# Kernel optimization log

Hardware: AMD Instinct MI355X
Metric: run time of the kernel (lower is better)

## Reference

```python
import jax, jax.numpy as jnp
import numpy as np

H = 64  # lstm hidden

def _lstm_scan(xs, h0, c0, wih, whh, bih, bhh):
    # xs: [T,B,D]; torch gate order i,f,g,o
    def step(carry, xt):
        h, c = carry
        gates = xt @ wih.T + h @ whh.T + bih + bhh
        i, f, g, o = jnp.split(gates, 4, axis=-1)
        c = jax.nn.sigmoid(f) * c + jax.nn.sigmoid(i) * jnp.tanh(g)
        h = jax.nn.sigmoid(o) * jnp.tanh(c)
        return (h, c), h
    (h, c), hs = jax.lax.scan(step, (h0, c0), xs)
    return hs, h, c


def setup_inputs() -> dict:
    key = jax.random.key(0)
    ks = jax.random.split(key, 32)
    r = lambda i, shape: (jax.random.normal(ks[i], shape, jnp.float32) * 0.05)
    B, T = 2048, 128
    inp = {
        "x": jax.random.normal(ks[0], (B, T, 37), jnp.float32),
        "enc_lin_w": r(1, (64, 37)), "enc_lin_b": r(2, (64,)),
        "enc_wih_f": r(3, (4 * H, 64)), "enc_whh_f": r(4, (4 * H, H)),
        "enc_bih_f": r(5, (4 * H,)), "enc_bhh_f": r(6, (4 * H,)),
        "enc_wih_b": r(7, (4 * H, 64)), "enc_whh_b": r(8, (4 * H, H)),
        "enc_bih_b": r(9, (4 * H,)), "enc_bhh_b": r(10, (4 * H,)),
        "att1_w": r(11, (32, 192)), "att1_b": r(12, (32,)),
        "att2_w": r(13, (1, 32)), "att2_b": r(14, (1,)),
        "dec_wih": r(15, (4 * H, 128)), "dec_whh": r(16, (4 * H, H)),
        "dec_bih": r(17, (4 * H,)), "dec_bhh": r(18, (4 * H,)),
        "dec_lin_w": r(19, (11, H)), "dec_lin_b": r(20, (11,)),
        "output_len": 10,
    }
    return inp


def reference(x, enc_lin_w, enc_lin_b,
              enc_wih_f, enc_whh_f, enc_bih_f, enc_bhh_f,
              enc_wih_b, enc_whh_b, enc_bih_b, enc_bhh_b,
              att1_w, att1_b, att2_w, att2_b,
              dec_wih, dec_whh, dec_bih, dec_bhh,
              dec_lin_w, dec_lin_b, output_len):
    B, T, _ = x.shape
    # ---- Encoder: linear -> relu -> BiLSTM ----
    e = jax.nn.relu(x @ enc_lin_w.T + enc_lin_b)          # [B,T,64]
    xs = jnp.transpose(e, (1, 0, 2))                       # [T,B,64]
    z = jnp.zeros((B, H), x.dtype)
    hf, _, _ = _lstm_scan(xs, z, z, enc_wih_f, enc_whh_f, enc_bih_f, enc_bhh_f)
    hb, _, _ = _lstm_scan(xs[::-1], z, z, enc_wih_b, enc_whh_b, enc_bih_b, enc_bhh_b)
    feats = jnp.concatenate([hf, hb[::-1]], axis=-1)       # [T,B,128]
    feats = jnp.transpose(feats, (1, 0, 2))                # [B,T,128]

    # ---- Decoder loop with (degenerate) additive attention ----
    def dec_step(carry, _):
        h, c = carry
        h_rep = jnp.broadcast_to(h[:, None, :], (B, T, H))
        fin = jnp.concatenate([feats, h_rep], axis=-1)     # [B,T,192]
        a = jnp.tanh(fin @ att1_w.T + att1_b)              # [B,T,32]
        s = a @ att2_w.T + att2_b                          # [B,T,1]
        scores = jax.nn.softmax(s, axis=-1)                # all ones (faithful to source)
        fd = jnp.sum(feats * scores, axis=1)               # [B,128]
        gates = fd @ dec_wih.T + h @ dec_whh.T + dec_bih + dec_bhh
        i, f, g, o = jnp.split(gates, 4, axis=-1)
        c = jax.nn.sigmoid(f) * c + jax.nn.sigmoid(i) * jnp.tanh(g)
        h = jax.nn.sigmoid(o) * jnp.tanh(c)
        out = jax.nn.softmax(h @ dec_lin_w.T + dec_lin_b, axis=-1)  # [B,11]
        return (h, c), out

    (_, _), outs = jax.lax.scan(dec_step, (z, z), None, length=output_len)
    return jnp.transpose(outs, (1, 0, 2))                  # [B,output_len,11]
```

## Files before the change

### kernel.cpp

```cpp
#include <hip/hip_runtime.h>


typedef _Float16 f16;
typedef f16 f16x8 __attribute__((ext_vector_type(8)));
typedef f16 f16x4 __attribute__((ext_vector_type(4)));
typedef float f32x4 __attribute__((ext_vector_type(4)));

#define MFMA16(a, b, c) __builtin_amdgcn_mfma_f32_16x16x32_f16(a, b, c, 0, 0, 0)

#define NLOG2E  -1.4426950408889634f
#define N2LOG2E -2.8853900817779268f

__device__ __forceinline__ float rcp_(float x) { return __builtin_amdgcn_rcpf(x); }
__device__ __forceinline__ float ex2_(float x) { return __builtin_amdgcn_exp2f(x); }
__device__ __forceinline__ float sigf(float x) { return 1.f / (1.f + __expf(-x)); }
__device__ __forceinline__ float tanhf_fast(float x) {
  float e = __expf(2.f * x);
  return 1.f - 2.f / (e + 1.f);
}


#define TC 8
__global__ __launch_bounds__(256) void enc_linear_k(
    const float* __restrict__ x, const float* __restrict__ w1,
    const float* __restrict__ b1, f16* __restrict__ efrag) {
  const int bg = blockIdx.x;
  const int tc = blockIdx.y;
  const int tid = threadIdx.x;
  const int w = tid >> 6, l = tid & 63;
  const int rho = l & 15, c = l >> 4;

  __shared__ float xls[16][8 * 37 + 1];
  __shared__ float ldsw[64 * 37];
  __shared__ __align__(16) f16 fstage[TC][2][64][8];

  for (int i = tid; i < 64 * 37; i += 256) ldsw[i] = w1[i];
#pragma unroll
  for (int rr = 0; rr < 4; rr++) {
    const int r = w * 4 + rr;
    const float* src = x + ((size_t)(bg * 16 + r) * 128 + tc * TC) * 37;
    for (int e = l; e < 296; e += 64) xls[r][e] = src[e];
  }
  __syncthreads();

  f16x8 a0, a1;
  {
    const float* pw = ldsw + (16 * w + rho) * 37;
#pragma unroll
    for (int i = 0; i < 8; i++) a0[i] = (f16)pw[8 * c + i];
#pragma unroll
    for (int i = 0; i < 8; i++) a1[i] = (f16)((c == 0 && i < 5) ? pw[32 + i] : 0.f);
  }
  f32x4 bias;
#pragma unroll
  for (int r = 0; r < 4; r++) bias[r] = b1[16 * w + 4 * c + r];

#pragma unroll
  for (int tl = 0; tl < TC; tl++) {
    const float* px = &xls[rho][tl * 37];
    f16x8 xb0, xb1;
#pragma unroll
    for (int i = 0; i < 8; i++) xb0[i] = (f16)px[8 * c + i];
#pragma unroll
    for (int i = 0; i < 8; i++) xb1[i] = (f16)((c == 0 && i < 5) ? px[32 + i] : 0.f);
    f32x4 acc = bias;
    acc = MFMA16(a0, xb0, acc);
    acc = MFMA16(a1, xb1, acc);
    f16x4 pk;
#pragma unroll
    for (int r = 0; r < 4; r++) pk[r] = (f16)fmaxf(acc[r], 0.f);
    const int d0 = 16 * w + 4 * c;
    *(f16x4*)&fstage[tl][w >> 1][rho | (((d0 >> 3) & 3) << 4)][d0 & 7] = pk;
  }
  __syncthreads();

  const float4* srcf = (const float4*)fstage;
  float4* dstf = (float4*)efrag;
  for (int i = tid; i < TC * 2 * 64; i += 256) {
    const int tl = i >> 7, rest = i & 127;
    dstf[((size_t)((tc * TC + tl) * 128 + bg) * 2) * 64 + rest] = srcf[i];
  }
}

__global__ __launch_bounds__(512, 2) void bilstm_k(
    const f16* __restrict__ efrag,
    const float* __restrict__ wih_f, const float* __restrict__ whh_f,
    const float* __restrict__ bih_f, const float* __restrict__ bhh_f,
    const float* __restrict__ wih_b, const float* __restrict__ whh_b,
    const float* __restrict__ bih_b, const float* __restrict__ bhh_b,
    float* __restrict__ fd) {
  const int bid = blockIdx.x;
  const int dir = bid >> 7;
  const int bg = bid & 127;
  const int tid = threadIdx.x;
  const int w = tid >> 6, l = tid & 63;
  const int rho = l & 15, c = l >> 4;
  const int gate = rho & 3, uoff = rho >> 2;

  const float* wih = dir ? wih_b : wih_f;
  const float* whh = dir ? whh_b : whh_f;
  const float* bih = dir ? bih_b : bih_f;
  const float* bhh = dir ? bhh_b : bhh_f;

  __shared__ __align__(16) f16 hbuf[2][2][64][8];
  {
    int* hz = (int*)hbuf;
    for (int i = tid; i < (int)(sizeof(hbuf) / 4); i += 512) hz[i] = 0;
  }

  const float sA = (gate == 2) ? N2LOG2E : NLOG2E;

  f16x8 aih[2][2], ahh[2][2];
#pragma unroll
  for (int q = 0; q < 2; q++) {
    const int m = 2 * w + q;
    const int n = gate * 64 + 4 * m + uoff;
#pragma unroll
    for (int ks = 0; ks < 2; ks++) {
      const float* p1 = wih + n * 64 + ks * 32 + c * 8;
      const float* p2 = whh + n * 64 + ks * 32 + c * 8;
      f16x8 v1, v2;
#pragma unroll
      for (int i = 0; i < 8; i++) {
        v1[i] = (f16)(p1[i] * sA);
        v2[i] = (f16)(p2[i] * sA);
      }
      aih[q][ks] = v1;
      ahh[q][ks] = v2;
    }
  }
  f32x4 bias[2];
#pragma unroll
  for (int q = 0; q < 2; q++) {
    const int j = 8 * w + 4 * q + c;
#pragma unroll
    for (int r = 0; r < 4; r++) {
      const float sr = (r == 2) ? N2LOG2E : NLOG2E;
      bias[q][r] = (bih[64 * r + j] + bhh[64 * r + j]) * sr;
    }
  }

  const f16x8* eb = (const f16x8*)efrag;
#define EIDX(t) (((size_t)(((dir ? 127 - (t) : (t)) * 128) + bg) * 2) * 64 + l)
  f16x8 ec0 = eb[EIDX(0)], ec1 = eb[EIDX(0) + 64];
  f16x8 e10 = eb[EIDX(1)], e11 = eb[EIDX(1) + 64];
  f16x8 e20 = eb[EIDX(2)], e21 = eb[EIDX(2) + 64];

  float cst[2] = {0.f, 0.f};
  float hs[2] = {0.f, 0.f};

  __syncthreads();

#pragma unroll 4
  for (int t = 0; t < 128; t++) {
    const int cur = t & 1;
    const int t3 = (t + 3 < 128) ? t + 3 : 127;
    const f16x8 ld0 = eb[EIDX(t3)];
    const f16x8 ld1 = eb[EIDX(t3) + 64];

    f16x8 h0 = *(const f16x8*)&hbuf[cur][0][l][0];
    f16x8 h1 = *(const f16x8*)&hbuf[cur][1][l][0];
#pragma unroll
    for (int q = 0; q < 2; q++) {
      f32x4 a = bias[q];
      a = MFMA16(aih[q][0], ec0, a);
      a = MFMA16(aih[q][1], ec1, a);
      a = MFMA16(ahh[q][0], h0, a);
      a = MFMA16(ahh[q][1], h1, a);
      const float ig = rcp_(1.f + ex2_(a[0]));
      const float fg = rcp_(1.f + ex2_(a[1]));
      const float gg = 2.f * rcp_(1.f + ex2_(a[2])) - 1.f;
      const float og = rcp_(1.f + ex2_(a[3]));
      cst[q] = fg * cst[q] + ig * gg;
      const float th = 2.f * rcp_(1.f + ex2_(cst[q] * N2LOG2E)) - 1.f;
      const float h = og * th;
      hs[q] += h;
      const int j = 8 * w + 4 * q + c;
      hbuf[cur ^ 1][j >> 5][rho | (((j >> 3) & 3) << 4)][j & 7] = (f16)h;
    }
    ec0 = e10; ec1 = e11;
    e10 = e20; e11 = e21;
    e20 = ld0; e21 = ld1;
    asm volatile("s_waitcnt lgkmcnt(0)\n\ts_barrier" ::: "memory");
  }
#undef EIDX
#pragma unroll
  for (int q = 0; q < 2; q++) {
    const int j = 8 * w + 4 * q + c;
    fd[(size_t)(bg * 16 + rho) * 128 + dir * 64 + j] = hs[q];
  }
}

__global__ __launch_bounds__(256) void decoder_k(
    const float* __restrict__ fd,
    const float* __restrict__ dwih, const float* __restrict__ dwhh,
    const float* __restrict__ dbih, const float* __restrict__ dbhh,
    const float* __restrict__ dlw, const float* __restrict__ dlb,
    const int* __restrict__ outlen_p, float* __restrict__ out) {
  const int b0 = blockIdx.x * 16;
  const int tid = threadIdx.x;
  const int w = tid >> 6, l = tid & 63;
  const int rho = l & 15, c = l >> 4;
  const int gate = rho & 3, uoff = rho >> 2;
  const int outlen = *outlen_p;

  __shared__ __align__(16) f16 hbuf[2][2][64][8];
  __shared__ float h32[64][16];
  __shared__ float ldslw[11 * 64];
  __shared__ float ldslb[16];
  __shared__ float lg[16][16];

  {
    int* hz = (int*)hbuf;
    for (int i = tid; i < (int)(sizeof(hbuf) / 4); i += 256) hz[i] = 0;
  }
  for (int i = tid; i < 704; i += 256) ldslw[i] = dlw[i];
  if (tid < 16) ldslb[tid] = (tid < 11) ? dlb[tid] : 0.f;

  f16x8 awhh[4][2];
  f32x4 acc0[4];
  {
    f16x8 bfd[4];
#pragma unroll
    for (int ks = 0; ks < 4; ks++) {
      const float* p = fd + (size_t)(b0 + rho) * 128 + ks * 32 + c * 8;
      f16x8 v;
#pragma unroll
      for (int i = 0; i < 8; i++) v[i] = (f16)p[i];
      bfd[ks] = v;
    }
#pragma unroll
    for (int q = 0; q < 4; q++) {
      const int m = 4 * w + q;
      const int n = gate * 64 + 4 * m + uoff;
      f32x4 a;
      const int j = 16 * w + 4 * q + c;
#pragma unroll
      for (int r = 0; r < 4; r++) a[r] = dbih[64 * r + j] + dbhh[64 * r + j];
#pragma unroll
      for (int ks = 0; ks < 4; ks++) {
        const float* p = dwih + n * 128 + ks * 32 + c * 8;
        f16x8 v;
#pragma unroll
        for (int i = 0; i < 8; i++) v[i] = (f16)p[i];
        a = MFMA16(v, bfd[ks], a);
      }
      acc0[q] = a;
#pragma unroll
      for (int ks = 0; ks < 2; ks++) {
        const float* p = dwhh + n * 64 + ks * 32 + c * 8;
        f16x8 v;
#pragma unroll
        for (int i = 0; i < 8; i++) v[i] = (f16)p[i];
        awhh[q][ks] = v;
      }
    }
  }
  float cst[4] = {0.f, 0.f, 0.f, 0.f};
  __syncthreads();

  for (int s = 0; s < outlen; s++) {
    const int cur = s & 1;
    f16x8 h0 = *(const f16x8*)&hbuf[cur][0][l][0];
    f16x8 h1 = *(const f16x8*)&hbuf[cur][1][l][0];
#pragma unroll
    for (int q = 0; q < 4; q++) {
      f32x4 a = acc0[q];
      a = MFMA16(awhh[q][0], h0, a);
      a = MFMA16(awhh[q][1], h1, a);
      const float ig = sigf(a[0]);
      const float fg = sigf(a[1]);
      const float gg = tanhf_fast(a[2]);
      const float og = sigf(a[3]);
      cst[q] = fg * cst[q] + ig * gg;
      const float h = og * tanhf_fast(cst[q]);
      const int j = 16 * w + 4 * q + c;
      hbuf[cur ^ 1][j >> 5][rho | (((j >> 3) & 3) << 4)][j & 7] = (f16)h;
      h32[j][rho] = h;
    }
    __syncthreads();
    const int b = tid >> 4, o = tid & 15;
    float logit = 0.f;
    if (o < 11) {
      logit = ldslb[o];
      for (int jj = 0; jj < 64; jj++) logit += h32[jj][b] * ldslw[o * 64 + jj];
      lg[b][o] = logit;
    }
    __syncthreads();
    if (o < 11) {
      float mx = lg[b][0];
      for (int k = 1; k < 11; k++) mx = fmaxf(mx, lg[b][k]);
      float sum = 0.f;
      for (int k = 0; k < 11; k++) sum += __expf(lg[b][k] - mx);
      out[(size_t)(b0 + b) * outlen * 11 + (size_t)s * 11 + o] =
          __expf(logit - mx) / sum;
    }
    __syncthreads();
  }
}

extern "C" void kernel_launch(void* const* d_in, const int* in_sizes, int n_in,
                              void* d_out, int out_size, void* d_ws, size_t ws_size,
                              hipStream_t stream) {
  const float* x = (const float*)d_in[0];
  const float* w1 = (const float*)d_in[1];
  const float* b1 = (const float*)d_in[2];
  const float* wih_f = (const float*)d_in[3];
  const float* whh_f = (const float*)d_in[4];
  const float* bih_f = (const float*)d_in[5];
  const float* bhh_f = (const float*)d_in[6];
  const float* wih_b = (const float*)d_in[7];
  const float* whh_b = (const float*)d_in[8];
  const float* bih_b = (const float*)d_in[9];
  const float* bhh_b = (const float*)d_in[10];
  const float* dwih = (const float*)d_in[15];
  const float* dwhh = (const float*)d_in[16];
  const float* dbih = (const float*)d_in[17];
  const float* dbhh = (const float*)d_in[18];
  const float* dlw = (const float*)d_in[19];
  const float* dlb = (const float*)d_in[20];
  const int* outlen = (const int*)d_in[21];
  float* out = (float*)d_out;

  f16* efrag = (f16*)d_ws;
  float* fd = (float*)((char*)d_ws + (size_t)33554432);

  hipLaunchKernelGGL(enc_linear_k, dim3(128, 16), dim3(256), 0, stream,
                     x, w1, b1, efrag);
  hipLaunchKernelGGL(bilstm_k, dim3(256), dim3(512), 0, stream,
                     efrag, wih_f, whh_f, bih_f, bhh_f,
                     wih_b, whh_b, bih_b, bhh_b, fd);
  hipLaunchKernelGGL(decoder_k, dim3(128), dim3(256), 0, stream,
                     fd, dwih, dwhh, dbih, dbhh, dlw, dlb, outlen, out);
}
```

Baseline: 136.6 us.

## Fuse encoder linear into BiLSTM kernel with producer warps feeding LDS

Removes the separate encoder-linear kernel and its fp16 global intermediate. The fused kernel stages each batch group's full input slab in LDS. Four extra warps compute the linear+ReLU projection for step t+1 into a double-buffered LDS tile while eight LSTM warps consume step t. The LSTM gate MFMAs are also split into two independent accumulation chains to shorten the dependency chain. The costs are a large up-front LDS fill, higher LDS use per block that may reduce occupancy, and a scalar tail for the five leftover input features.

```diff
diff --git a/kernel.cpp b/kernel.cpp
--- a/kernel.cpp
+++ b/kernel.cpp
@@ -19,71 +19,9 @@
   return 1.f - 2.f / (e + 1.f);
 }
 
-
-#define TC 8
-__global__ __launch_bounds__(256) void enc_linear_k(
+__global__ __launch_bounds__(768, 3) void bilstm_fused_k(
     const float* __restrict__ x, const float* __restrict__ w1,
-    const float* __restrict__ b1, f16* __restrict__ efrag) {
-  const int bg = blockIdx.x;
-  const int tc = blockIdx.y;
-  const int tid = threadIdx.x;
-  const int w = tid >> 6, l = tid & 63;
-  const int rho = l & 15, c = l >> 4;
-
-  __shared__ float xls[16][8 * 37 + 1];
-  __shared__ float ldsw[64 * 37];
-  __shared__ __align__(16) f16 fstage[TC][2][64][8];
-
-  for (int i = tid; i < 64 * 37; i += 256) ldsw[i] = w1[i];
-#pragma unroll
-  for (int rr = 0; rr < 4; rr++) {
-    const int r = w * 4 + rr;
-    const float* src = x + ((size_t)(bg * 16 + r) * 128 + tc * TC) * 37;
-    for (int e = l; e < 296; e += 64) xls[r][e] = src[e];
-  }
-  __syncthreads();
-
-  f16x8 a0, a1;
-  {
-    const float* pw = ldsw + (16 * w + rho) * 37;
-#pragma unroll
-    for (int i = 0; i < 8; i++) a0[i] = (f16)pw[8 * c + i];
-#pragma unroll
-    for (int i = 0; i < 8; i++) a1[i] = (f16)((c == 0 && i < 5) ? pw[32 + i] : 0.f);
-  }
-  f32x4 bias;
-#pragma unroll
-  for (int r = 0; r < 4; r++) bias[r] = b1[16 * w + 4 * c + r];
-
-#pragma unroll
-  for (int tl = 0; tl < TC; tl++) {
-    const float* px = &xls[rho][tl * 37];
-    f16x8 xb0, xb1;
-#pragma unroll
-    for (int i = 0; i < 8; i++) xb0[i] = (f16)px[8 * c + i];
-#pragma unroll
-    for (int i = 0; i < 8; i++) xb1[i] = (f16)((c == 0 && i < 5) ? px[32 + i] : 0.f);
-    f32x4 acc = bias;
-    acc = MFMA16(a0, xb0, acc);
-    acc = MFMA16(a1, xb1, acc);
-    f16x4 pk;
-#pragma unroll
-    for (int r = 0; r < 4; r++) pk[r] = (f16)fmaxf(acc[r], 0.f);
-    const int d0 = 16 * w + 4 * c;
-    *(f16x4*)&fstage[tl][w >> 1][rho | (((d0 >> 3) & 3) << 4)][d0 & 7] = pk;
-  }
-  __syncthreads();
-
-  const float4* srcf = (const float4*)fstage;
-  float4* dstf = (float4*)efrag;
-  for (int i = tid; i < TC * 2 * 64; i += 256) {
-    const int tl = i >> 7, rest = i & 127;
-    dstf[((size_t)((tc * TC + tl) * 128 + bg) * 2) * 64 + rest] = srcf[i];
-  }
-}
-
-__global__ __launch_bounds__(512, 2) void bilstm_k(
-    const f16* __restrict__ efrag,
+    const float* __restrict__ b1,
     const float* __restrict__ wih_f, const float* __restrict__ whh_f,
     const float* __restrict__ bih_f, const float* __restrict__ bhh_f,
     const float* __restrict__ wih_b, const float* __restrict__ whh_b,
@@ -97,97 +35,146 @@
   const int rho = l & 15, c = l >> 4;
   const int gate = rho & 3, uoff = rho >> 2;
 
-  const float* wih = dir ? wih_b : wih_f;
-  const float* whh = dir ? whh_b : whh_f;
-  const float* bih = dir ? bih_b : bih_f;
-  const float* bhh = dir ? bhh_b : bhh_f;
-
+  __shared__ __align__(16) f16 xfrag[128][64][8];
   __shared__ __align__(16) f16 hbuf[2][2][64][8];
+  __shared__ __align__(16) f16 ebuf[2][2][64][8];
+  __shared__ f16 xtail[128][16][5];
+
   {
+    const float4* xsrc = (const float4*)(x + (size_t)bg * 16 * 4736);
+    for (int cidx = tid; cidx < 18944; cidx += 768) {
+      const float4 v = xsrc[cidx];
+      const int bb = ((cidx >> 5) * 56680) >> 21;
+      const int f0 = (cidx - bb * 1184) * 4;
+      const float vv[4] = {v.x, v.y, v.z, v.w};
+#pragma unroll
+      for (int e = 0; e < 4; e++) {
+        const int f = f0 + e;
+        const int tt = (f * 56680) >> 21;
+        const int kk = f - tt * 37;
+        const f16 hv = (f16)vv[e];
+        if (kk < 32) xfrag[tt][bb | (((kk >> 3) & 3) << 4)][kk & 7] = hv;
+        else xtail[tt][bb][kk - 32] = hv;
+      }
+    }
     int* hz = (int*)hbuf;
-    for (int i = tid; i < (int)(sizeof(hbuf) / 4); i += 512) hz[i] = 0;
-  }
-
-  const float sA = (gate == 2) ? N2LOG2E : NLOG2E;
-
+    for (int i = tid; i < 1024; i += 768) hz[i] = 0;
+  }
+
+  const bool enc = (w < 4);
+  f16x8 w1a = {};
+  float w1t[4][5];
+  f32x4 eb0 = {};
   f16x8 aih[2][2], ahh[2][2];
-#pragma unroll
-  for (int q = 0; q < 2; q++) {
-    const int m = 2 * w + q;
-    const int n = gate * 64 + 4 * m + uoff;
-#pragma unroll
-    for (int ks = 0; ks < 2; ks++) {
-      const float* p1 = wih + n * 64 + ks * 32 + c * 8;
-      const float* p2 = whh + n * 64 + ks * 32 + c * 8;
-      f16x8 v1, v2;
-#pragma unroll
-      for (int i = 0; i < 8; i++) {
-        v1[i] = (f16)(p1[i] * sA);
-        v2[i] = (f16)(p2[i] * sA);
-      }
-      aih[q][ks] = v1;
-      ahh[q][ks] = v2;
-    }
-  }
   f32x4 bias[2];
-#pragma unroll
-  for (int q = 0; q < 2; q++) {
-    const int j = 8 * w + 4 * q + c;
+
+  if (enc) {
+    const float* pw = w1 + (16 * w + rho) * 37;
+#pragma unroll
+    for (int i = 0; i < 8; i++) w1a[i] = (f16)pw[8 * c + i];
 #pragma unroll
     for (int r = 0; r < 4; r++) {
-      const float sr = (r == 2) ? N2LOG2E : NLOG2E;
-      bias[q][r] = (bih[64 * r + j] + bhh[64 * r + j]) * sr;
-    }
-  }
-
-  const f16x8* eb = (const f16x8*)efrag;
-#define EIDX(t) (((size_t)(((dir ? 127 - (t) : (t)) * 128) + bg) * 2) * 64 + l)
-  f16x8 ec0 = eb[EIDX(0)], ec1 = eb[EIDX(0) + 64];
-  f16x8 e10 = eb[EIDX(1)], e11 = eb[EIDX(1) + 64];
-  f16x8 e20 = eb[EIDX(2)], e21 = eb[EIDX(2) + 64];
+      const float* pt = w1 + (16 * w + 4 * c + r) * 37 + 32;
+#pragma unroll
+      for (int i = 0; i < 5; i++) w1t[r][i] = pt[i];
+      eb0[r] = b1[16 * w + 4 * c + r];
+    }
+  } else {
+    const int wr = w - 4;
+    const float* wih = dir ? wih_b : wih_f;
+    const float* whh = dir ? whh_b : whh_f;
+    const float* bih = dir ? bih_b : bih_f;
+    const float* bhh = dir ? bhh_b : bhh_f;
+    const float sA = (gate == 2) ? N2LOG2E : NLOG2E;
+#pragma unroll
+    for (int q = 0; q < 2; q++) {
+      const int m = 2 * wr + q;
+      const int n = gate * 64 + 4 * m + uoff;
+#pragma unroll
+      for (int ks = 0; ks < 2; ks++) {
+        const float* p1 = wih + n * 64 + ks * 32 + c * 8;
+        const float* p2 = whh + n * 64 + ks * 32 + c * 8;
+        f16x8 v1, v2;
+#pragma unroll
+        for (int i = 0; i < 8; i++) {
+          v1[i] = (f16)(p1[i] * sA);
+          v2[i] = (f16)(p2[i] * sA);
+        }
+        aih[q][ks] = v1;
+        ahh[q][ks] = v2;
+      }
+      const int j = 8 * wr + 4 * q + c;
+#pragma unroll
+      for (int r = 0; r < 4; r++) {
+        const float sr = (r == 2) ? N2LOG2E : NLOG2E;
+        bias[q][r] = (bih[64 * r + j] + bhh[64 * r + j]) * sr;
+      }
+    }
+  }
+
+  auto enc_build = [&](int tm, int buf) {
+    const f16x8 xb0 = *(const f16x8*)&xfrag[tm][l][0];
+    float xt[5];
+#pragma unroll
+    for (int i = 0; i < 5; i++) xt[i] = (float)xtail[tm][rho][i];
+    f32x4 ea = MFMA16(w1a, xb0, eb0);
+#pragma unroll
+    for (int r = 0; r < 4; r++)
+#pragma unroll
+      for (int i = 0; i < 5; i++) ea[r] += w1t[r][i] * xt[i];
+    f16x4 pk;
+#pragma unroll
+    for (int r = 0; r < 4; r++) pk[r] = (f16)fmaxf(ea[r], 0.f);
+    const int d0 = 16 * w + 4 * c;
+    *(f16x4*)&ebuf[buf][w >> 1][rho | (((d0 >> 3) & 3) << 4)][d0 & 7] = pk;
+  };
+
+  __syncthreads();
+
+  if (enc) enc_build(dir ? 127 : 0, 0);
+  __syncthreads();
 
   float cst[2] = {0.f, 0.f};
   float hs[2] = {0.f, 0.f};
-
-  __syncthreads();
-
-#pragma unroll 4
+  const f32x4 z4 = {0.f, 0.f, 0.f, 0.f};
+
   for (int t = 0; t < 128; t++) {
-    const int cur = t & 1;
-    const int t3 = (t + 3 < 128) ? t + 3 : 127;
-    const f16x8 ld0 = eb[EIDX(t3)];
-    const f16x8 ld1 = eb[EIDX(t3) + 64];
-
-    f16x8 h0 = *(const f16x8*)&hbuf[cur][0][l][0];
-    f16x8 h1 = *(const f16x8*)&hbuf[cur][1][l][0];
+    const int cur = t & 1, nxt = cur ^ 1;
+    if (enc) {
+      if (t + 1 < 128) enc_build(dir ? 126 - t : t + 1, nxt);
+    } else {
+      const f16x8 e0 = *(const f16x8*)&ebuf[cur][0][l][0];
+      const f16x8 e1 = *(const f16x8*)&ebuf[cur][1][l][0];
+      const f16x8 h0 = *(const f16x8*)&hbuf[cur][0][l][0];
+      const f16x8 h1 = *(const f16x8*)&hbuf[cur][1][l][0];
+#pragma unroll
+      for (int q = 0; q < 2; q++) {
+        f32x4 a1 = MFMA16(aih[q][0], e0, bias[q]);
+        f32x4 a2 = MFMA16(aih[q][1], e1, z4);
+        a1 = MFMA16(ahh[q][0], h0, a1);
+        a2 = MFMA16(ahh[q][1], h1, a2);
+        const f32x4 a = a1 + a2;
+        const float ig = rcp_(1.f + ex2_(a[0]));
+        const float fg = rcp_(1.f + ex2_(a[1]));
+        const float gg = 2.f * rcp_(1.f + ex2_(a[2])) - 1.f;
+        const float og = rcp_(1.f + ex2_(a[3]));
+        cst[q] = fg * cst[q] + ig * gg;
+        const float th = 2.f * rcp_(1.f + ex2_(cst[q] * N2LOG2E)) - 1.f;
+        const float h = og * th;
+        hs[q] += h;
+        const int j = 8 * (w - 4) + 4 * q + c;
+        hbuf[nxt][j >> 5][rho | (((j >> 3) & 3) << 4)][j & 7] = (f16)h;
+      }
+    }
+    asm volatile("s_waitcnt lgkmcnt(0)\n\ts_barrier" ::: "memory");
+  }
+
+  if (!enc) {
 #pragma unroll
     for (int q = 0; q < 2; q++) {
-      f32x4 a = bias[q];
-      a = MFMA16(aih[q][0], ec0, a);
-      a = MFMA16(aih[q][1], ec1, a);
-      a = MFMA16(ahh[q][0], h0, a);
-      a = MFMA16(ahh[q][1], h1, a);
-      const float ig = rcp_(1.f + ex2_(a[0]));
-      const float fg = rcp_(1.f + ex2_(a[1]));
-      const float gg = 2.f * rcp_(1.f + ex2_(a[2])) - 1.f;
-      const float og = rcp_(1.f + ex2_(a[3]));
-      cst[q] = fg * cst[q] + ig * gg;
-      const float th = 2.f * rcp_(1.f + ex2_(cst[q] * N2LOG2E)) - 1.f;
-      const float h = og * th;
-      hs[q] += h;
-      const int j = 8 * w + 4 * q + c;
-      hbuf[cur ^ 1][j >> 5][rho | (((j >> 3) & 3) << 4)][j & 7] = (f16)h;
-    }
-    ec0 = e10; ec1 = e11;
-    e10 = e20; e11 = e21;
-    e20 = ld0; e21 = ld1;
-    asm volatile("s_waitcnt lgkmcnt(0)\n\ts_barrier" ::: "memory");
-  }
-#undef EIDX
-#pragma unroll
-  for (int q = 0; q < 2; q++) {
-    const int j = 8 * w + 4 * q + c;
-    fd[(size_t)(bg * 16 + rho) * 128 + dir * 64 + j] = hs[q];
+      const int j = 8 * (w - 4) + 4 * q + c;
+      fd[(size_t)(bg * 16 + rho) * 128 + dir * 64 + j] = hs[q];
+    }
   }
 }
 
@@ -322,13 +309,10 @@
   const int* outlen = (const int*)d_in[21];
   float* out = (float*)d_out;
 
-  f16* efrag = (f16*)d_ws;
-  float* fd = (float*)((char*)d_ws + (size_t)33554432);
-
-  hipLaunchKernelGGL(enc_linear_k, dim3(128, 16), dim3(256), 0, stream,
-                     x, w1, b1, efrag);
-  hipLaunchKernelGGL(bilstm_k, dim3(256), dim3(512), 0, stream,
-                     efrag, wih_f, whh_f, bih_f, bhh_f,
+  float* fd = (float*)d_ws;
+
+  hipLaunchKernelGGL(bilstm_fused_k, dim3(256), dim3(768), 0, stream,
+                     x, w1, b1, wih_f, whh_f, bih_f, bhh_f,
                      wih_b, whh_b, bih_b, bhh_b, fd);
   hipLaunchKernelGGL(decoder_k, dim3(128), dim3(256), 0, stream,
                      fd, dwih, dwhh, dbih, dbhh, dlw, dlb, outlen, out);
```

New measurement: 142.3 us. +4.2%, slower.

## Restructure encoder linear tiling and split LSTM MFMA accumulation chains

Applied to the files above, without the earlier changes.

The encoder linear kernel now processes 32 timesteps per block instead of 8, loading x with float4 reads into an f16 LDS tile. Each wave keeps all four weight fragments in registers and computes the 5-element K tail with scalar FMAs instead of a second mostly-zero MFMA. In the BiLSTM recurrence, the four dependent MFMAs per gate group are split into two independent chains that are summed at the end, shortening the serial dependency on the critical recurrent path. The trade-offs are fewer encoder blocks (less parallelism), more register pressure, and an extra vector add per step.

```diff
diff --git a/kernel.cpp b/kernel.cpp
--- a/kernel.cpp
+++ b/kernel.cpp
@@ -20,7 +20,7 @@
 }
 
 
-#define TC 8
+#define XSTRIDE 1304
 __global__ __launch_bounds__(256) void enc_linear_k(
     const float* __restrict__ x, const float* __restrict__ w1,
     const float* __restrict__ b1, f16* __restrict__ efrag) {
@@ -30,55 +30,77 @@
   const int w = tid >> 6, l = tid & 63;
   const int rho = l & 15, c = l >> 4;
 
-  __shared__ float xls[16][8 * 37 + 1];
-  __shared__ float ldsw[64 * 37];
-  __shared__ __align__(16) f16 fstage[TC][2][64][8];
-
-  for (int i = tid; i < 64 * 37; i += 256) ldsw[i] = w1[i];
-#pragma unroll
-  for (int rr = 0; rr < 4; rr++) {
-    const int r = w * 4 + rr;
-    const float* src = x + ((size_t)(bg * 16 + r) * 128 + tc * TC) * 37;
-    for (int e = l; e < 296; e += 64) xls[r][e] = src[e];
+  __shared__ f16 xls[16 * XSTRIDE];
+  __shared__ __align__(16) f16 fstage[32][2][64][8];
+
+  {
+    const float4* xsrc =
+        (const float4*)(x + ((size_t)(bg * 16) * 128 + tc * 32) * 37);
+    for (int cidx = tid; cidx < 16 * 296; cidx += 256) {
+      const int r = cidx / 296;
+      const int f4 = cidx - r * 296;
+      const float4 v = xsrc[(size_t)r * 1184 + f4];
+      const float vv[4] = {v.x, v.y, v.z, v.w};
+      const int f0 = f4 * 4;
+#pragma unroll
+      for (int e = 0; e < 4; e++) {
+        const int f = f0 + e;
+        const int t = (f * 1772) >> 16;
+        const int k = f - t * 37;
+        xls[r * XSTRIDE + t * 40 + k] = (f16)vv[e];
+      }
+    }
+  }
+
+  f16x8 w1a[4];
+  float w1t[4][4][5];
+  f32x4 ebias[4];
+#pragma unroll
+  for (int m = 0; m < 4; m++) {
+    const float* pw = w1 + (16 * m + rho) * 37;
+    f16x8 v0;
+#pragma unroll
+    for (int i = 0; i < 8; i++) v0[i] = (f16)pw[8 * c + i];
+    w1a[m] = v0;
+#pragma unroll
+    for (int r = 0; r < 4; r++) {
+      const float* pt = w1 + (16 * m + 4 * c + r) * 37 + 32;
+#pragma unroll
+      for (int i = 0; i < 5; i++) w1t[m][r][i] = pt[i];
+      ebias[m][r] = b1[16 * m + 4 * c + r];
+    }
   }
   __syncthreads();
 
-  f16x8 a0, a1;
-  {
-    const float* pw = ldsw + (16 * w + rho) * 37;
-#pragma unroll
-    for (int i = 0; i < 8; i++) a0[i] = (f16)pw[8 * c + i];
-#pragma unroll
-    for (int i = 0; i < 8; i++) a1[i] = (f16)((c == 0 && i < 5) ? pw[32 + i] : 0.f);
-  }
-  f32x4 bias;
-#pragma unroll
-  for (int r = 0; r < 4; r++) bias[r] = b1[16 * w + 4 * c + r];
-
-#pragma unroll
-  for (int tl = 0; tl < TC; tl++) {
-    const float* px = &xls[rho][tl * 37];
-    f16x8 xb0, xb1;
-#pragma unroll
-    for (int i = 0; i < 8; i++) xb0[i] = (f16)px[8 * c + i];
-#pragma unroll
-    for (int i = 0; i < 8; i++) xb1[i] = (f16)((c == 0 && i < 5) ? px[32 + i] : 0.f);
-    f32x4 acc = bias;
-    acc = MFMA16(a0, xb0, acc);
-    acc = MFMA16(a1, xb1, acc);
-    f16x4 pk;
-#pragma unroll
-    for (int r = 0; r < 4; r++) pk[r] = (f16)fmaxf(acc[r], 0.f);
-    const int d0 = 16 * w + 4 * c;
-    *(f16x4*)&fstage[tl][w >> 1][rho | (((d0 >> 3) & 3) << 4)][d0 & 7] = pk;
+#pragma unroll
+  for (int ti = 0; ti < 8; ti++) {
+    const int tl = 8 * w + ti;
+    const f16* px = xls + rho * XSTRIDE + tl * 40;
+    const f16x8 xb0 = *(const f16x8*)(px + 8 * c);
+    float xt[5];
+#pragma unroll
+    for (int i = 0; i < 5; i++) xt[i] = (float)px[32 + i];
+#pragma unroll
+    for (int m = 0; m < 4; m++) {
+      f32x4 ea = MFMA16(w1a[m], xb0, ebias[m]);
+#pragma unroll
+      for (int r = 0; r < 4; r++)
+#pragma unroll
+        for (int i = 0; i < 5; i++) ea[r] += w1t[m][r][i] * xt[i];
+      f16x4 pk;
+#pragma unroll
+      for (int r = 0; r < 4; r++) pk[r] = (f16)fmaxf(ea[r], 0.f);
+      const int d0 = 16 * m + 4 * c;
+      *(f16x4*)&fstage[tl][m >> 1][rho | (((d0 >> 3) & 3) << 4)][d0 & 7] = pk;
+    }
   }
   __syncthreads();
 
   const float4* srcf = (const float4*)fstage;
   float4* dstf = (float4*)efrag;
-  for (int i = tid; i < TC * 2 * 64; i += 256) {
+  for (int i = tid; i < 4096; i += 256) {
     const int tl = i >> 7, rest = i & 127;
-    dstf[((size_t)((tc * TC + tl) * 128 + bg) * 2) * 64 + rest] = srcf[i];
+    dstf[((size_t)((tc * 32 + tl) * 128 + bg) * 2) * 64 + rest] = srcf[i];
   }
 }
 
@@ -148,6 +170,7 @@
 
   float cst[2] = {0.f, 0.f};
   float hs[2] = {0.f, 0.f};
+  const f32x4 z4 = {0.f, 0.f, 0.f, 0.f};
 
   __syncthreads();
 
@@ -162,11 +185,11 @@
     f16x8 h1 = *(const f16x8*)&hbuf[cur][1][l][0];
 #pragma unroll
     for (int q = 0; q < 2; q++) {
-      f32x4 a = bias[q];
-      a = MFMA16(aih[q][0], ec0, a);
-      a = MFMA16(aih[q][1], ec1, a);
-      a = MFMA16(ahh[q][0], h0, a);
-      a = MFMA16(ahh[q][1], h1, a);
+      f32x4 a1 = MFMA16(aih[q][0], ec0, bias[q]);
+      f32x4 a2 = MFMA16(aih[q][1], ec1, z4);
+      a1 = MFMA16(ahh[q][0], h0, a1);
+      a2 = MFMA16(ahh[q][1], h1, a2);
+      const f32x4 a = a1 + a2;
       const float ig = rcp_(1.f + ex2_(a[0]));
       const float fg = rcp_(1.f + ex2_(a[1]));
       const float gg = 2.f * rcp_(1.f + ex2_(a[2])) - 1.f;
@@ -325,7 +348,7 @@
   f16* efrag = (f16*)d_ws;
   float* fd = (float*)((char*)d_ws + (size_t)33554432);
 
-  hipLaunchKernelGGL(enc_linear_k, dim3(128, 16), dim3(256), 0, stream,
+  hipLaunchKernelGGL(enc_linear_k, dim3(128, 4), dim3(256), 0, stream,
                      x, w1, b1, efrag);
   hipLaunchKernelGGL(bilstm_k, dim3(256), dim3(512), 0, stream,
                      efrag, wih_f, whh_f, bih_f, bhh_f,
```

New measurement: 129.5 us. -5.2%, faster.
